# Kernel optimization log

Measured on AMD Instinct MI355X. Metric: run time of the kernel, lower is better.

Reference implementation:

```python
import jax, jax.numpy as jnp
import numpy as np
from jax import lax

RATIOS = (0.5, 1.0, 2.0)
SCALES = (8, 16, 32)
STRIDE = 16
N_ANCHOR = 9
N_PRE = 6000      # eval-mode n_pre_nms
N_POST = 300      # eval-mode n_post_nms
NMS_THRESH = 0.7
MIN_SIZE = 16.0


def _anchor_base():
    rows = []
    for r in RATIOS:
        for s in SCALES:
            h = STRIDE * s * np.sqrt(r)
            w = STRIDE * s * np.sqrt(1.0 / r)
            c = STRIDE / 2.0
            rows.append([c - h / 2.0, c - w / 2.0, c + h / 2.0, c + w / 2.0])
    return jnp.asarray(np.array(rows, np.float32))  # [9,4]


def _all_anchors(hh, ww):
    ab = _anchor_base()
    sy, sx = jnp.meshgrid(jnp.arange(hh) * STRIDE, jnp.arange(ww) * STRIDE, indexing='ij')
    shift = jnp.stack([sy.ravel(), sx.ravel(), sy.ravel(), sx.ravel()], axis=1).astype(jnp.float32)
    return (shift[:, None, :] + ab[None, :, :]).reshape(-1, 4)  # [hh*ww*9, 4]


def _conv(x, w, b, pad):
    y = lax.conv_general_dilated(x, w, (1, 1), ((pad, pad), (pad, pad)),
                                 dimension_numbers=('NCHW', 'OIHW', 'NCHW'))
    return y + b[None, :, None, None]


def _loc2bbox(anchor, loc):
    ah = anchor[:, 2] - anchor[:, 0]
    aw = anchor[:, 3] - anchor[:, 1]
    acy = anchor[:, 0] + 0.5 * ah
    acx = anchor[:, 1] + 0.5 * aw
    dy, dx, dh, dw = loc[:, 0], loc[:, 1], loc[:, 2], loc[:, 3]
    cy = dy * ah + acy
    cx = dx * aw + acx
    h = jnp.exp(dh) * ah
    w = jnp.exp(dw) * aw
    return jnp.stack([cy - 0.5 * h, cx - 0.5 * w, cy + 0.5 * h, cx + 0.5 * w], axis=1)


def _iou_matrix(boxes):
    tl = jnp.maximum(boxes[:, None, :2], boxes[None, :, :2])
    br = jnp.minimum(boxes[:, None, 2:], boxes[None, :, 2:])
    wh = jnp.clip(br - tl, 0.0)
    inter = wh[..., 0] * wh[..., 1]
    area = (boxes[:, 2] - boxes[:, 0]) * (boxes[:, 3] - boxes[:, 1])
    return inter / (area[:, None] + area[None, :] - inter + 1e-9)


def _nms_keep(boxes, valid):
    # boxes sorted by descending score; sequential greedy NMS via fori_loop.
    iou = _iou_matrix(boxes)
    idx = jnp.arange(boxes.shape[0])

    def body(i, keep):
        sup = keep[i] & (iou[i] > NMS_THRESH) & (idx > i)
        return keep & ~sup

    return lax.fori_loop(0, boxes.shape[0], body, valid)


def _proposals(loc, fg_score, anchors, img_h, img_w):
    boxes = _loc2bbox(anchors, loc)
    boxes = jnp.clip(boxes, 0.0, jnp.array([img_h, img_w, img_h, img_w], jnp.float32))
    hs = boxes[:, 2] - boxes[:, 0]
    ws = boxes[:, 3] - boxes[:, 1]
    valid = (hs >= MIN_SIZE) & (ws >= MIN_SIZE)
    score = jnp.where(valid, fg_score, -jnp.inf)
    topv, topi = lax.top_k(score, N_PRE)          # pre-NMS selection by score
    boxes = boxes[topi]
    keep = _nms_keep(boxes, topv > -jnp.inf)
    # compact first N_POST kept boxes (score order), zero-padded if fewer.
    rank = jnp.cumsum(keep) - 1
    pos = jnp.where(keep & (rank < N_POST), rank, N_POST)
    return jnp.zeros((N_POST + 1, 4), boxes.dtype).at[pos].set(boxes)[:N_POST]


def setup_inputs():
    key = jax.random.key(0)
    ks = jax.random.split(key, 4)
    C = 512
    return {
        'feature_map': jax.random.normal(ks[0], (2, C, 64, 64), jnp.float32),
        'conv1_w': jax.random.normal(ks[1], (C, C, 3, 3), jnp.float32) * 0.01,
        'conv1_b': jnp.zeros((C,), jnp.float32),
        'score_w': jax.random.normal(ks[2], (N_ANCHOR * 2, C, 1, 1), jnp.float32) * 0.01,
        'score_b': jnp.zeros((N_ANCHOR * 2,), jnp.float32),
        'loc_w': jax.random.normal(ks[3], (N_ANCHOR * 4, C, 1, 1), jnp.float32) * 0.01,
        'loc_b': jnp.zeros((N_ANCHOR * 4,), jnp.float32),
        'img_h': 1024,
        'img_w': 1024,
    }


def reference(feature_map, conv1_w, conv1_b, score_w, score_b, loc_w, loc_b, img_h, img_w):
    n, _, hh, ww = feature_map.shape
    h = jax.nn.relu(_conv(feature_map, conv1_w, conv1_b, 1))
    rpn_locs = _conv(h, loc_w, loc_b, 0).transpose(0, 2, 3, 1).reshape(n, -1, 4)
    scores_raw = _conv(h, score_w, score_b, 0).transpose(0, 2, 3, 1)  # [n,hh,ww,18]
    sm = jax.nn.softmax(scores_raw.reshape(n, hh, ww, N_ANCHOR, 2), axis=4)
    rpn_fg_scores = sm[..., 1].reshape(n, -1)
    rpn_scores = scores_raw.reshape(n, -1, 2)
    anchors = _all_anchors(hh, ww)
    rois = jax.vmap(lambda l, s: _proposals(l, s, anchors, img_h, img_w))(rpn_locs, rpn_fg_scores)
    roi_indices = jnp.repeat(jnp.arange(n, dtype=jnp.int32), N_POST)
    return rpn_locs, rpn_scores, rois.reshape(-1, 4), roi_indices, anchors
```

## Files before the change

### kernel.cpp

```cpp
#include <hip/hip_runtime.h>
#include <cmath>

#define NANCH 36864
#define NPRE 6000
#define NPOST 300

#define LOCS_OFF   0
#define SCORES_OFF 294912
#define ROIS_OFF   442368
#define RIDX_OFF   444768
#define ANCH_OFF   445368

#define WT_OFF      0ull
#define WTH_OFF     0ull
#define WTL_OFF     4718592ull
#define PREFIX_OFF  2097152ull
#define PREFIXM_OFF 2621440ull
#define SORTED_OFF  3145728ull
#define MASK_OFF    0ull
#define H_OFF       9437184ull
#define BOXES_OFF   26214400ull
#define W54_OFF     26214400ull
#define KEYS_OFF    27394048ull
#define HIST_OFF    27983872ull
#define SKEYS_OFF   28631168ull
#define SBOXES_OFF  28727168ull
#define VMASK_OFF   29033856ull
#define XTH_OFF     29360128ull
#define XTL_OFF     37748736ull
#define WS_NEED_MFMA 46137344ull

typedef _Float16 half8 __attribute__((ext_vector_type(8)));
typedef float floatx4 __attribute__((ext_vector_type(4)));

__device__ __forceinline__ void load_lds16(const float* g, float* l) {
#if __has_builtin(__builtin_amdgcn_global_load_lds)
  __builtin_amdgcn_global_load_lds(
      (const __attribute__((address_space(1))) void*)g,
      (__attribute__((address_space(3))) void*)l, 16, 0, 0);
#else
  int lane = threadIdx.x & 63;
  float4 v = *(const float4*)g;
  *(float4*)((char*)l + lane * 16) = v;
#endif
}

__device__ __forceinline__ void load_lds16g(const void* g, void* l) {
#if __has_builtin(__builtin_amdgcn_global_load_lds)
  __builtin_amdgcn_global_load_lds(
      (const __attribute__((address_space(1))) void*)g,
      (__attribute__((address_space(3))) void*)l, 16, 0, 0);
#else
  int lane = threadIdx.x & 63;
  float4 v = *(const float4*)g;
  *(float4*)((char*)l + lane * 16) = v;
#endif
}

__global__ __launch_bounds__(1024) void prep_kernel(
    const float* __restrict__ w, float* __restrict__ wt,
    const float* __restrict__ lw, const float* __restrict__ sw,
    float* __restrict__ w54p) {
  __shared__ float lds[9][32][33];
  if (blockIdx.x < 256) {
    int tx = threadIdx.x & 31;
    int ty = threadIdx.x >> 5;
    int ci0 = (blockIdx.x & 15) * 32;
    int co0 = (blockIdx.x >> 4) * 32;
    const float* src = w + ((size_t)(co0 + ty) * 512 + (ci0 + tx)) * 9;
#pragma unroll
    for (int k = 0; k < 9; k++) lds[k][tx][ty] = src[k];
    __syncthreads();
#pragma unroll
    for (int k = 0; k < 9; k++) {
      wt[((size_t)k * 512 + (ci0 + ty)) * 512 + co0 + tx] = lds[k][ty][tx];
    }
  } else {
    int t = (blockIdx.x - 256) * 1024 + threadIdx.x;
    int k = t >> 6, co = t & 63;
    float v = 0.f;
    if (co < 36) v = lw[(size_t)co * 512 + k];
    else if (co < 54) v = sw[(size_t)(co - 36) * 512 + k];
    w54p[t] = v;
  }
}

__global__ __launch_bounds__(1024) void prep16_kernel(
    const float* __restrict__ w, _Float16* __restrict__ wth,
    _Float16* __restrict__ wtl, const float* __restrict__ lw,
    const float* __restrict__ sw, float* __restrict__ w54p) {
  if (blockIdx.x < 256) {
    int tx = threadIdx.x & 31;
    int ty = threadIdx.x >> 5;
    int ci0 = (blockIdx.x & 15) * 32;
    int co0 = (blockIdx.x >> 4) * 32;
    const float* src = w + ((size_t)(co0 + ty) * 512 + (ci0 + tx)) * 9;
    size_t o = (size_t)(co0 + ty) * 512 + (ci0 + tx);
#pragma unroll
    for (int k = 0; k < 9; k++) {
      float v = src[k];
      _Float16 h = (_Float16)v;
      _Float16 l = (_Float16)((v - (float)h) * 1024.f);
      wth[(size_t)k * 262144 + o] = h;
      wtl[(size_t)k * 262144 + o] = l;
    }
  } else {
    int t = (blockIdx.x - 256) * 1024 + threadIdx.x;
    int k = t >> 6, co = t & 63;
    float v = 0.f;
    if (co < 36) v = lw[(size_t)co * 512 + k];
    else if (co < 54) v = sw[(size_t)(co - 36) * 512 + k];
    w54p[t] = v;
  }
}

__global__ __launch_bounds__(256) void prepx_kernel(
    const float* __restrict__ x, _Float16* __restrict__ xth,
    _Float16* __restrict__ xtl) {
  __shared__ float xs[32][65];
  int b = blockIdx.x;
  int cs = b & 15, ny = b >> 4;
  int n = ny >> 6, y = ny & 63;
  int tid = threadIdx.x;
  const float* xb = x + ((size_t)n << 21) + (y << 6);
#pragma unroll
  for (int p = 0; p < 8; p++) {
    int c = p * 4 + (tid >> 6);
    xs[c][tid & 63] = xb[((size_t)(cs * 32 + c) << 12) + (tid & 63)];
  }
  __syncthreads();
  int px = tid >> 2, cq = (tid & 3) * 8;
  unsigned int hw[4], lw2[4];
#pragma unroll
  for (int j = 0; j < 4; j++) {
    float v0 = xs[cq + 2 * j][px], v1 = xs[cq + 2 * j + 1][px];
    _Float16 h0 = (_Float16)v0, h1 = (_Float16)v1;
    _Float16 l0 = (_Float16)((v0 - (float)h0) * 1024.f);
    _Float16 l1 = (_Float16)((v1 - (float)h1) * 1024.f);
    hw[j] = (unsigned int)__builtin_bit_cast(unsigned short, h0) |
            ((unsigned int)__builtin_bit_cast(unsigned short, h1) << 16);
    lw2[j] = (unsigned int)__builtin_bit_cast(unsigned short, l0) |
             ((unsigned int)__builtin_bit_cast(unsigned short, l1) << 16);
  }
  size_t o = (size_t)b * 2048 + (size_t)px * 32 + cq;
  uint4 hv; hv.x = hw[0]; hv.y = hw[1]; hv.z = hw[2]; hv.w = hw[3];
  uint4 lv; lv.x = lw2[0]; lv.y = lw2[1]; lv.z = lw2[2]; lv.w = lw2[3];
  *(uint4*)(xth + o) = hv;
  *(uint4*)(xtl + o) = lv;
}

__global__ __launch_bounds__(256, 3) void conv1_mfma_kernel(
    const _Float16* __restrict__ xth, const _Float16* __restrict__ xtl,
    const _Float16* __restrict__ wth, const _Float16* __restrict__ wtl,
    const float* __restrict__ bias, float* __restrict__ hout) {
  __shared__ __align__(16) _Float16 sXh[6336];
  __shared__ __align__(16) _Float16 sXl[6336];
  __shared__ __align__(16) _Float16 sWh[4096];
  __shared__ __align__(16) _Float16 sWl[4096];
  int mb = blockIdx.x;
  int n = mb >> 6, y = mb & 63;
  int co0 = blockIdx.y << 7;
  int tid = threadIdx.x;
  int wv = tid >> 6, lane = tid & 63;
  int m15 = lane & 15, g = lane >> 4;

  floatx4 accm[2][4], accl[2][4];
#pragma unroll
  for (int ct = 0; ct < 2; ct++)
#pragma unroll
    for (int pt = 0; pt < 4; pt++) {
      accm[ct][pt] = (floatx4){0.f, 0.f, 0.f, 0.f};
      accl[ct][pt] = (floatx4){0.f, 0.f, 0.f, 0.f};
    }

  for (int t2 = tid; t2 < 3168; t2 += 256) {
    ((unsigned int*)sXh)[t2] = 0u;
    ((unsigned int*)sXl)[t2] = 0u;
  }
  __syncthreads();

  bool yv0 = (y > 0), yv2 = (y < 63);

  for (int cs = 0; cs < 16; cs++) {
    {
      int base = wv * 6;
#pragma unroll
      for (int i = 0; i < 6; i++) {
        int idx = base + i;
        int yr = idx >> 3, rem = idx & 7;
        int part = rem >> 2, d = rem & 3;
        int ys = y + yr - 1;
        if (ys >= 0 && ys < 64) {
          const _Float16* s =
              (part ? xtl : xth) +
              ((((size_t)(n * 64 + ys)) * 16 + cs) << 11) + (d << 9) +
              ((lane >> 2) << 5) + ((lane & 3) << 3);
          _Float16* dst = (part ? sXl : sXh) + yr * 2112 + 32 + (d << 9);
          load_lds16g(s, dst);
        }
      }
    }
    int ci0 = cs << 5;
    int p = wv >> 1, hf = wv & 1;
    const _Float16* wbase =
        (p ? wtl : wth) + (size_t)co0 * 512 + ci0 +
        ((size_t)(hf * 64 + (lane >> 2))) * 512 + ((lane & 3) << 3);
    _Float16* wdst0 = (p ? sWl : sWh) + (hf << 11);
#pragma unroll
    for (int tap = 0; tap < 9; tap++) {
      int ky = tap / 3;
      int kx = tap - ky * 3;
      if (ky == 0 && !yv0) continue;
      if (ky == 2 && !yv2) continue;
      const _Float16* ws = wbase + (size_t)tap * 262144;
#pragma unroll
      for (int d = 0; d < 4; d++)
        load_lds16g(ws + (size_t)d * 8192, wdst0 + (d << 9));
      __syncthreads();
      half8 Ah[2], Al[2], Bh[4], Bl[4];
#pragma unroll
      for (int ct = 0; ct < 2; ct++) {
        int ao = ((wv << 5) + (ct << 4) + m15) * 32 + (g << 3);
        Ah[ct] = *(const half8*)(sWh + ao);
        Al[ct] = *(const half8*)(sWl + ao);
      }
#pragma unroll
      for (int pt = 0; pt < 4; pt++) {
        int bo = ky * 2112 + ((pt << 4) + m15 + kx) * 32 + (g << 3);
        Bh[pt] = *(const half8*)(sXh + bo);
        Bl[pt] = *(const half8*)(sXl + bo);
      }
#pragma unroll
      for (int ct = 0; ct < 2; ct++)
#pragma unroll
        for (int pt = 0; pt < 4; pt++) {
          accm[ct][pt] = __builtin_amdgcn_mfma_f32_16x16x32_f16(
              Ah[ct], Bh[pt], accm[ct][pt], 0, 0, 0);
          accl[ct][pt] = __builtin_amdgcn_mfma_f32_16x16x32_f16(
              Ah[ct], Bl[pt], accl[ct][pt], 0, 0, 0);
          accl[ct][pt] = __builtin_amdgcn_mfma_f32_16x16x32_f16(
              Al[ct], Bh[pt], accl[ct][pt], 0, 0, 0);
        }
      __syncthreads();
    }
  }

#pragma unroll
  for (int ct = 0; ct < 2; ct++)
#pragma unroll
    for (int pt = 0; pt < 4; pt++) {
#pragma unroll
      for (int r = 0; r < 4; r++) {
        int co = co0 + (wv << 5) + (ct << 4) + (g << 2) + r;
        float v = accm[ct][pt][r] + accl[ct][pt][r] * 0.0009765625f +
                  bias[co];
        hout[((size_t)(n * 512 + co) << 12) + (y << 6) + (pt << 4) + m15] =
            fmaxf(v, 0.f);
      }
    }
}

__global__ __launch_bounds__(256) void conv1_kernel(
    const float* __restrict__ x, const float* __restrict__ wt,
    const float* __restrict__ bias, float* __restrict__ hout) {
  __shared__ __align__(16) float smem[10752];
  int mb = blockIdx.x;
  int n = mb >> 6, y = mb & 63;
  int co0 = blockIdx.y << 7;
  int tid = threadIdx.x;
  int team = tid >> 7;
  int tl = tid & 127;
  int cibase = team << 8;
  float* Asb = smem + team * 768;
  float* Bsb = smem + 1536 + team * 4608;
  int tx = tl & 7, ty = tl >> 3;
  int x0 = tx << 3;

  float acc[8][8];
#pragma unroll
  for (int j = 0; j < 8; j++)
#pragma unroll
    for (int i = 0; i < 8; i++) acc[j][i] = 0.f;

  const float* xb = x + ((size_t)n << 21);

  if (y == 0) {
    for (int t2 = tl; t2 < 256; t2 += 128) Asb[t2] = 0.f;
  }
  if (y == 63) {
    for (int t2 = tl; t2 < 256; t2 += 128) Asb[512 + t2] = 0.f;
  }

  int wv = tl >> 6;
  int lane = tl & 63;
  int lrow = lane >> 5;
  int lcol = (lane & 31) << 2;
  int aci = lane >> 4;
  int aoff = (lane & 15) << 2;

  for (int cc = 0; cc < 256; cc += 4) {
    int ci0 = cibase + cc;
    for (int yr = wv; yr < 3; yr += 2) {
      int ys = y + yr - 1;
      if (ys >= 0 && ys < 64) {
        const float* g =
            xb + (((size_t)(ci0 + aci)) << 12) + (ys << 6) + aoff;
        load_lds16(g, &Asb[yr << 8]);
      }
    }
    for (int i = 0; i < 9; i++) {
      int r0 = i * 4 + wv * 2;
      int row = r0 + lrow;
      int kk = row >> 2, ci = row & 3;
      const float* g = wt + (((size_t)(kk << 9)) + ci0 + ci) * 512 + co0 + lcol;
      load_lds16(g, &Bsb[r0 << 7]);
    }
    __syncthreads();
    for (int k = 0; k < 4; k++) {
#pragma unroll
      for (int ky = 0; ky < 3; ky++) {
        const float* arr = &Asb[((ky << 2) + k) << 6];
        float w10[10];
        w10[0] = (tx == 0) ? 0.f : arr[x0 - 1];
        float4 a0 = *(const float4*)&arr[x0];
        float4 a1 = *(const float4*)&arr[x0 + 4];
        w10[1] = a0.x; w10[2] = a0.y; w10[3] = a0.z; w10[4] = a0.w;
        w10[5] = a1.x; w10[6] = a1.y; w10[7] = a1.z; w10[8] = a1.w;
        w10[9] = (tx == 7) ? 0.f : arr[x0 + 8];
#pragma unroll
        for (int kx = 0; kx < 3; kx++) {
          int kk = ky * 3 + kx;
          const float* br = &Bsb[(((kk << 2) + k) << 7) + (ty << 3)];
          float4 b0 = *(const float4*)br;
          float4 b1 = *(const float4*)(br + 4);
          float bb[8] = {b0.x, b0.y, b0.z, b0.w, b1.x, b1.y, b1.z, b1.w};
#pragma unroll
          for (int j = 0; j < 8; j++)
#pragma unroll
            for (int dx = 0; dx < 8; dx++)
              acc[j][dx] = fmaf(w10[kx + dx], bb[j], acc[j][dx]);
        }
      }
    }
    __syncthreads();
  }

  if (team == 1) {
#pragma unroll
    for (int j = 0; j < 8; j++) {
      *(float4*)&smem[tl * 68 + (j << 3)] = *(float4*)&acc[j][0];
      *(float4*)&smem[tl * 68 + (j << 3) + 4] = *(float4*)&acc[j][4];
    }
  }
  __syncthreads();
  if (team == 0) {
#pragma unroll
    for (int j = 0; j < 8; j++) {
      int co = co0 + (ty << 3) + j;
      float bv = bias[co];
      float4 p0 = *(float4*)&smem[tl * 68 + (j << 3)];
      float4 p1 = *(float4*)&smem[tl * 68 + (j << 3) + 4];
      float4 v0, v1;
      v0.x = fmaxf((acc[j][0] + p0.x) + bv, 0.f);
      v0.y = fmaxf((acc[j][1] + p0.y) + bv, 0.f);
      v0.z = fmaxf((acc[j][2] + p0.z) + bv, 0.f);
      v0.w = fmaxf((acc[j][3] + p0.w) + bv, 0.f);
      v1.x = fmaxf((acc[j][4] + p1.x) + bv, 0.f);
      v1.y = fmaxf((acc[j][5] + p1.y) + bv, 0.f);
      v1.z = fmaxf((acc[j][6] + p1.z) + bv, 0.f);
      v1.w = fmaxf((acc[j][7] + p1.w) + bv, 0.f);
      float* o = &hout[(((size_t)(n * 512 + co)) << 12) + (y << 6) + x0];
      *(float4*)o = v0;
      *(float4*)(o + 4) = v1;
    }
  }
}

__global__ __launch_bounds__(256) void heads_kernel(
    const float* __restrict__ h, const float* __restrict__ w54p,
    const float* __restrict__ loc_b, const float* __restrict__ score_b,
    float* __restrict__ out) {
  __shared__ __align__(16) float hs[32 * 64];
  __shared__ __align__(16) float wsd[32 * 64];
  __shared__ float sacc[64 * 65];
  int n = blockIdx.x >> 6;
  int p0 = (blockIdx.x & 63) << 6;
  int tid = threadIdx.x;
  int txp = tid & 63;
  int tw = tid >> 6;
  float acc[16];
#pragma unroll
  for (int j = 0; j < 16; j++) acc[j] = 0.f;
  const float* hb = h + ((size_t)n * 512) * 4096 + p0;
  for (int k0 = 0; k0 < 512; k0 += 32) {
    for (int t = tid; t < 512; t += 256) {
      int r = t >> 4, l = (t & 15) << 2;
      *(float4*)&hs[(r << 6) + l] =
          *(const float4*)&hb[(((size_t)(k0 + r)) << 12) + l];
      *(float4*)&wsd[(r << 6) + l] =
          *(const float4*)&w54p[((k0 + r) << 6) + l];
    }
    __syncthreads();
    for (int k = 0; k < 32; k++) {
      float hv = hs[(k << 6) + txp];
      const float* wr = &wsd[(k << 6) + (tw << 4)];
#pragma unroll
      for (int u = 0; u < 4; u++) {
        float4 wv = *(const float4*)(wr + (u << 2));
        acc[u * 4 + 0] = fmaf(hv, wv.x, acc[u * 4 + 0]);
        acc[u * 4 + 1] = fmaf(hv, wv.y, acc[u * 4 + 1]);
        acc[u * 4 + 2] = fmaf(hv, wv.z, acc[u * 4 + 2]);
        acc[u * 4 + 3] = fmaf(hv, wv.w, acc[u * 4 + 3]);
      }
    }
    __syncthreads();
  }
#pragma unroll
  for (int j = 0; j < 16; j++) sacc[(tw * 16 + j) * 65 + txp] = acc[j];
  __syncthreads();
  for (int t = tid; t < 64 * 54; t += 256) {
    int p = t / 54, c = t - p * 54;
    float v = sacc[c * 65 + p];
    int gp = (n << 12) + p0 + p;
    if (c < 36) out[LOCS_OFF + (size_t)gp * 36 + c] = v + loc_b[c];
    else out[SCORES_OFF + (size_t)gp * 18 + (c - 36)] = v + score_b[c - 36];
  }
}

__global__ void decode_kernel(const float* __restrict__ out_ro,
                              const int* __restrict__ pimh,
                              const int* __restrict__ pimw,
                              float* __restrict__ boxes,
                              unsigned long long* __restrict__ keys,
                              unsigned int* __restrict__ hist,
                              float* __restrict__ out) {
  int t = blockIdx.x * 256 + threadIdx.x;
  int n = t / NANCH, k = t - n * NANCH;
  float imh = (float)pimh[0], imw = (float)pimw[0];

  int a = k % 9, pos = k / 9;
  int jj = pos & 63, ii = pos >> 6;
  int ridx = a / 3, sidx = a % 3;
  double r = (ridx == 0) ? 0.5 : ((ridx == 1) ? 1.0 : 2.0);
  double s = (sidx == 0) ? 8.0 : ((sidx == 1) ? 16.0 : 32.0);
  double ahh = 16.0 * s * sqrt(r);
  double aww = 16.0 * s * sqrt(1.0 / r);
  float b0 = (float)(8.0 - ahh / 2.0), b1 = (float)(8.0 - aww / 2.0);
  float b2 = (float)(8.0 + ahh / 2.0), b3 = (float)(8.0 + aww / 2.0);
  float sy = (float)(ii * 16), sx = (float)(jj * 16);
  float a0 = sy + b0, a1 = sx + b1, a2 = sy + b2, a3 = sx + b3;
  if (n == 0) {
    float* o = out + ANCH_OFF + (size_t)k * 4;
    o[0] = a0; o[1] = a1; o[2] = a2; o[3] = a3;
  }

  const float* loc = out_ro + LOCS_OFF + (size_t)t * 4;
  const float* sc = out_ro + SCORES_OFF + (size_t)t * 2;
  float ah = __fsub_rn(a2, a0), aw = __fsub_rn(a3, a1);
  float acy = __fadd_rn(a0, 0.5f * ah), acx = __fadd_rn(a1, 0.5f * aw);
  float dy = loc[0], dx = loc[1], dh = loc[2], dw = loc[3];
  float cy = __fadd_rn(__fmul_rn(dy, ah), acy);
  float cx = __fadd_rn(__fmul_rn(dx, aw), acx);
  float hh = __fmul_rn(expf(dh), ah);
  float ww = __fmul_rn(expf(dw), aw);
  float y1 = __fsub_rn(cy, 0.5f * hh), x1 = __fsub_rn(cx, 0.5f * ww);
  float y2 = __fadd_rn(cy, 0.5f * hh), x2 = __fadd_rn(cx, 0.5f * ww);
  y1 = fminf(fmaxf(y1, 0.f), imh); x1 = fminf(fmaxf(x1, 0.f), imw);
  y2 = fminf(fmaxf(y2, 0.f), imh); x2 = fminf(fmaxf(x2, 0.f), imw);
  bool valid = (__fsub_rn(y2, y1) >= 16.f) && (__fsub_rn(x2, x1) >= 16.f);
  float s0 = sc[0], s1 = sc[1];
  float m = fmaxf(s0, s1);
  float e0 = expf(__fsub_rn(s0, m)), e1 = expf(__fsub_rn(s1, m));
  float fg = __fdiv_rn(e1, __fadd_rn(e0, e1));
  float score = valid ? fg : -INFINITY;
  unsigned int u = __float_as_uint(score);
  unsigned int ord = (u & 0x80000000u) ? ~u : (u | 0x80000000u);
  unsigned long long key =
      ((unsigned long long)(~ord) << 16) | (unsigned long long)(k & 0xFFFF);
  float4 b4; b4.x = y1; b4.y = x1; b4.z = y2; b4.w = x2;
  *(float4*)(boxes + (size_t)t * 4) = b4;
  keys[t] = key;
  if (valid)
    atomicAdd(&hist[((size_t)n << 16) + (unsigned int)(key >> 32)], 1u);
}

__global__ __launch_bounds__(1024) void scanfull_kernel(
    const unsigned int* __restrict__ hist, unsigned int* __restrict__ prefix,
    unsigned int* __restrict__ prefix_mut) {
  int n = blockIdx.x;
  const uint4* h4 = (const uint4*)(hist + ((size_t)n << 16));
  uint4* pf4 = (uint4*)(prefix + ((size_t)n << 16));
  uint4* pm4 = (uint4*)(prefix_mut + ((size_t)n << 16));
  __shared__ unsigned int ps[1024];
  int tid = threadIdx.x;
  int base4 = tid << 4;
  uint4 vals[16];
  unsigned int s = 0;
#pragma unroll
  for (int i = 0; i < 16; i++) {
    vals[i] = h4[base4 + i];
    s += vals[i].x + vals[i].y + vals[i].z + vals[i].w;
  }
  ps[tid] = s;
  __syncthreads();
  for (int off = 1; off < 1024; off <<= 1) {
    unsigned int v = ps[tid];
    unsigned int add = (tid >= off) ? ps[tid - off] : 0u;
    __syncthreads();
    ps[tid] = v + add;
    __syncthreads();
  }
  unsigned int run = ps[tid] - s;
#pragma unroll
  for (int i = 0; i < 16; i++) {
    uint4 hv = vals[i];
    uint4 pv;
    pv.x = run; run += hv.x;
    pv.y = run; run += hv.y;
    pv.z = run; run += hv.z;
    pv.w = run; run += hv.w;
    pf4[base4 + i] = pv;
    pm4[base4 + i] = pv;
  }
}

__global__ void scatter_kernel(const unsigned long long* __restrict__ keys,
                               unsigned int* __restrict__ prefix_mut,
                               unsigned long long* __restrict__ sorted) {
  int t = blockIdx.x * 256 + threadIdx.x;
  int n = t / NANCH;
  unsigned long long key = keys[t];
  unsigned int b = (unsigned int)(key >> 32);
  if (b >= 0xFF80u) return;
  unsigned int pos = atomicAdd(&prefix_mut[((size_t)n << 16) + b], 1u);
  if (pos < 8192) sorted[((size_t)n << 13) + pos] = key;
}

__global__ void fixup_kernel(const unsigned long long* __restrict__ sorted,
                             const unsigned int* __restrict__ prefix,
                             const unsigned int* __restrict__ hist,
                             const float* __restrict__ boxes,
                             unsigned long long* __restrict__ skeys,
                             float* __restrict__ sboxes) {
  int t = blockIdx.x * 256 + threadIdx.x;
  int n = t / 7168;
  int s = t - n * 7168;
  const unsigned long long* srt = sorted + ((size_t)n << 13);
  unsigned long long key = srt[s];
  unsigned int hi = (unsigned int)(key >> 16);
  if (hi >= 0xFF800000u) {
    if (s < NPRE) skeys[(size_t)n * NPRE + s] = key;
    return;
  }
  unsigned int b = (unsigned int)(key >> 32);
  unsigned int st = prefix[((size_t)n << 16) + b];
  if (st >= (unsigned)NPRE) return;
  unsigned int cnt = hist[((size_t)n << 16) + b];
  unsigned int r = 0;
  if (cnt > 1) {
    for (unsigned int j = 0; j < cnt; j++) r += (srt[st + j] < key) ? 1u : 0u;
  }
  unsigned int pos = st + r;
  if (pos < (unsigned)NPRE) {
    skeys[(size_t)n * NPRE + pos] = key;
    int k = (int)(key & 0xFFFFull);
    float4 bx = *(const float4*)(boxes + (((size_t)n * NANCH) + k) * 4);
    *(float4*)(sboxes + ((size_t)n * NPRE + pos) * 4) = bx;
  }
}

__global__ __launch_bounds__(64) void nms_mask_kernel(
    const float* __restrict__ sboxes,
    const unsigned long long* __restrict__ skeys,
    unsigned long long* __restrict__ vmask,
    unsigned long long* __restrict__ mask) {
  int n = blockIdx.z;
  int ib = blockIdx.x, jb = blockIdx.y;
  if (jb < ib) return;
  int lane = threadIdx.x;
  __shared__ __align__(16) float jbox[64][4];
  int j = jb * 64 + lane;
  float4 bj4 = (j < NPRE)
                   ? *(const float4*)(sboxes + ((size_t)n * NPRE + j) * 4)
                   : float4{0.f, 0.f, 0.f, 0.f};
  *(float4*)jbox[lane] = bj4;
  __syncthreads();
  if (jb == ib) {
    int idx = ib * 64 + lane;
    bool ok = false;
    if (idx < NPRE) {
      unsigned int khi = (unsigned int)(skeys[(size_t)n * NPRE + idx] >> 16);
      ok = khi < 0xFF800000u;
    }
    unsigned long long m = __ballot(ok);
    if (lane == 0) vmask[(size_t)n * 94 + ib] = m;
  }
  int i = ib * 64 + lane;
  if (i >= NPRE) return;
  float4 bi = *(const float4*)(sboxes + ((size_t)n * NPRE + i) * 4);
  float ay1 = bi.x, ax1 = bi.y, ay2 = bi.z, ax2 = bi.w;
  float areaA = __fmul_rn(__fsub_rn(ay2, ay1), __fsub_rn(ax2, ax1));
  unsigned long long bits = 0ull;
#pragma unroll 8
  for (int l = 0; l < 64; l++) {
    float4 bj = *(const float4*)jbox[l];
    float ty1 = fmaxf(ay1, bj.x), tx1 = fmaxf(ax1, bj.y);
    float ty2 = fminf(ay2, bj.z), tx2 = fminf(ax2, bj.w);
    float wh0 = fmaxf(__fsub_rn(ty2, ty1), 0.f);
    float wh1 = fmaxf(__fsub_rn(tx2, tx1), 0.f);
    float inter = __fmul_rn(wh0, wh1);
    float areaB = __fmul_rn(__fsub_rn(bj.z, bj.x), __fsub_rn(bj.w, bj.y));
    float den = __fadd_rn(__fsub_rn(__fadd_rn(areaA, areaB), inter), 1e-9f);
    float iou = __fdiv_rn(inter, den);
    if (iou > 0.7f) bits |= (1ull << l);
  }
  mask[((size_t)n * NPRE + i) * 94 + jb] = bits;
}

__global__ __launch_bounds__(64) void nms_reduce_kernel(
    const unsigned long long* __restrict__ mask,
    const unsigned long long* __restrict__ vmask,
    const float* __restrict__ sboxes, float* __restrict__ out) {
  int n = blockIdx.x;
  int lane = threadIdx.x;
  __shared__ int kept[NPOST];
  __shared__ int s_count;

  unsigned long long rlo = ~vmask[(size_t)n * 94 + lane];
  unsigned long long rhi = (64 + lane < 94) ? ~vmask[(size_t)n * 94 + 64 + lane]
                                            : ~0ull;
  int count = 0;
  for (int c = 0; c < 94 && count < NPOST; c++) {
    unsigned long long curw =
        (c < 64) ? __shfl(rlo, c) : __shfl(rhi, c - 64);
    unsigned long long cand = ~curw;
    while (cand != 0ull && count < NPOST) {
      int b = __builtin_ctzll(cand);
      int i = c * 64 + b;
      if (lane == 0) kept[count] = i;
      count++;
      const unsigned long long* row = mask + ((size_t)n * NPRE + i) * 94;
      unsigned long long r0 = row[lane];
      unsigned long long r1 = (64 + lane < 94) ? row[64 + lane] : 0ull;
      rlo |= r0; rhi |= r1;
      curw = (c < 64) ? __shfl(rlo, c) : __shfl(rhi, c - 64);
      cand = ~curw;
      cand &= (b == 63) ? 0ull : (~0ull << (b + 1));
    }
  }
  if (lane == 0) s_count = count;
  __syncthreads();
  count = s_count;

  float* rois = out + ROIS_OFF + (size_t)n * NPOST * 4;
  float* ridx = out + RIDX_OFF + (size_t)n * NPOST;
  for (int s = lane; s < NPOST; s += 64) {
    float4 v = {0.f, 0.f, 0.f, 0.f};
    if (s < count) {
      int i = kept[s];
      v = *(const float4*)(sboxes + ((size_t)n * NPRE + i) * 4);
    }
    *(float4*)(rois + (size_t)s * 4) = v;
    ridx[s] = (float)n;
  }
}

extern "C" void kernel_launch(void* const* d_in, const int* in_sizes, int n_in,
                              void* d_out, int out_size, void* d_ws,
                              size_t ws_size, hipStream_t stream) {
  const float* feat = (const float*)d_in[0];
  const float* w1 = (const float*)d_in[1];
  const float* b1 = (const float*)d_in[2];
  const float* sw = (const float*)d_in[3];
  const float* sb = (const float*)d_in[4];
  const float* lw = (const float*)d_in[5];
  const float* lb = (const float*)d_in[6];
  const int* pimh = (const int*)d_in[7];
  const int* pimw = (const int*)d_in[8];
  float* out = (float*)d_out;
  char* ws = (char*)d_ws;

  float* wt = (float*)(ws + WT_OFF);
  _Float16* wth = (_Float16*)(ws + WTH_OFF);
  _Float16* wtl = (_Float16*)(ws + WTL_OFF);
  _Float16* xth = (_Float16*)(ws + XTH_OFF);
  _Float16* xtl = (_Float16*)(ws + XTL_OFF);
  float* w54p = (float*)(ws + W54_OFF);
  float* hbuf = (float*)(ws + H_OFF);
  float* boxes = (float*)(ws + BOXES_OFF);
  unsigned long long* keys = (unsigned long long*)(ws + KEYS_OFF);
  unsigned int* hist = (unsigned int*)(ws + HIST_OFF);
  unsigned int* prefix = (unsigned int*)(ws + PREFIX_OFF);
  unsigned int* prefix_mut = (unsigned int*)(ws + PREFIXM_OFF);
  unsigned long long* sorted = (unsigned long long*)(ws + SORTED_OFF);
  unsigned long long* skeys = (unsigned long long*)(ws + SKEYS_OFF);
  float* sboxes = (float*)(ws + SBOXES_OFF);
  unsigned long long* vmask = (unsigned long long*)(ws + VMASK_OFF);
  unsigned long long* nmask = (unsigned long long*)(ws + MASK_OFF);

  hipMemsetAsync(ws + HIST_OFF, 0, 524288, stream);
  hipMemsetAsync(ws + SORTED_OFF, 0xFF, 131072, stream);

  bool big = (ws_size >= WS_NEED_MFMA);
  if (big) {
    prep16_kernel<<<288, 1024, 0, stream>>>(w1, wth, wtl, lw, sw, w54p);
    prepx_kernel<<<2048, 256, 0, stream>>>(feat, xth, xtl);
    conv1_mfma_kernel<<<dim3(128, 4), 256, 0, stream>>>(xth, xtl, wth, wtl,
                                                        b1, hbuf);
  } else {
    prep_kernel<<<288, 1024, 0, stream>>>(w1, wt, lw, sw, w54p);
    conv1_kernel<<<dim3(128, 4), 256, 0, stream>>>(feat, wt, b1, hbuf);
  }
  heads_kernel<<<128, 256, 0, stream>>>(hbuf, w54p, lb, sb, out);
  decode_kernel<<<288, 256, 0, stream>>>(out, pimh, pimw, boxes, keys, hist,
                                         out);
  scanfull_kernel<<<2, 1024, 0, stream>>>(hist, prefix, prefix_mut);
  scatter_kernel<<<288, 256, 0, stream>>>(keys, prefix_mut, sorted);
  fixup_kernel<<<56, 256, 0, stream>>>(sorted, prefix, hist, boxes, skeys,
                                       sboxes);
  nms_mask_kernel<<<dim3(94, 94, 2), 64, 0, stream>>>(sboxes, skeys, vmask,
                                                      nmask);
  nms_reduce_kernel<<<2, 64, 0, stream>>>(nmask, vmask, sboxes, out);
}
```

Baseline: 631.8 us.

## Prefetch upcoming NMS mask rows speculatively in the sequential reduce loop

Rewrites the greedy NMS reduce loop so it keeps up to four candidate surviving boxes ahead and issues their suppression-row loads early. Candidates are found with wave ballots over the removed bitmask. Any speculative candidate that a newly kept box kills is recomputed and reloaded. The goal is to hide global-memory latency on the serial dependency chain of row loads, at the cost of extra ballot and shuffle work per step and occasional wasted loads.

New measurement: 769.9 us. 1.22x slower.

```diff
diff --git a/kernel.cpp b/kernel.cpp
--- a/kernel.cpp
+++ b/kernel.cpp
@@ -617,6 +617,61 @@
   mask[((size_t)n * NPRE + i) * 94 + jb] = bits;
 }
 
+#define QINV (1 << 30)
+
+__device__ __forceinline__ unsigned long long nms_word_at(
+    unsigned long long rlo, unsigned long long rhi, int w) {
+  unsigned long long lo = __shfl(rlo, w & 63);
+  unsigned long long hi = __shfl(rhi, (w - 64) & 63);
+  return (w < 64) ? lo : hi;
+}
+
+__device__ __forceinline__ int nms_next_alive(unsigned long long rlo,
+                                              unsigned long long rhi,
+                                              int lane, int pfrom) {
+  int w0 = pfrom >> 6, b0 = pfrom & 63;
+  unsigned long long mylo = ~rlo;
+  if (lane < w0) mylo = 0ull;
+  else if (lane == w0) mylo &= (~0ull << b0);
+  int l2 = lane + 64;
+  unsigned long long myhi = (l2 < 94) ? ~rhi : 0ull;
+  if (l2 < w0) myhi = 0ull;
+  else if (l2 == w0) myhi &= (~0ull << b0);
+  unsigned long long blo = __ballot(mylo != 0ull);
+  unsigned long long bhi = __ballot(myhi != 0ull);
+  int w;
+  unsigned long long wv;
+  if (blo) {
+    w = (int)__builtin_ctzll(blo);
+    wv = __shfl(mylo, w);
+  } else if (bhi) {
+    int wl = (int)__builtin_ctzll(bhi);
+    w = 64 + wl;
+    wv = __shfl(myhi, wl);
+  } else {
+    return QINV;
+  }
+  return (w << 6) + (int)__builtin_ctzll(wv);
+}
+
+__device__ __forceinline__ void nms_load_row(
+    const unsigned long long* __restrict__ mask, size_t nbase, int q,
+    int lane, unsigned long long& r0, unsigned long long& r1) {
+  if (q < QINV) {
+    const unsigned long long* row = mask + (nbase + (size_t)q) * 94;
+    r0 = row[lane];
+    r1 = (64 + lane < 94) ? row[64 + lane] : 0ull;
+  } else {
+    r0 = 0ull;
+    r1 = 0ull;
+  }
+}
+
+__device__ __forceinline__ bool nms_dead(unsigned long long rlo,
+                                         unsigned long long rhi, int q) {
+  return ((nms_word_at(rlo, rhi, q >> 6) >> (q & 63)) & 1ull) != 0ull;
+}
+
 __global__ __launch_bounds__(64) void nms_reduce_kernel(
     const unsigned long long* __restrict__ mask,
     const unsigned long long* __restrict__ vmask,
@@ -625,28 +680,49 @@
   int lane = threadIdx.x;
   __shared__ int kept[NPOST];
   __shared__ int s_count;
+  size_t nbase = (size_t)n * NPRE;
 
   unsigned long long rlo = ~vmask[(size_t)n * 94 + lane];
   unsigned long long rhi = (64 + lane < 94) ? ~vmask[(size_t)n * 94 + 64 + lane]
                                             : ~0ull;
+
+  int q0 = nms_next_alive(rlo, rhi, lane, 0);
+  int q1 = (q0 == QINV) ? QINV : nms_next_alive(rlo, rhi, lane, q0 + 1);
+  int q2 = (q1 == QINV) ? QINV : nms_next_alive(rlo, rhi, lane, q1 + 1);
+  int q3 = (q2 == QINV) ? QINV : nms_next_alive(rlo, rhi, lane, q2 + 1);
+  unsigned long long a0, c0, a1, c1, a2, c2, a3, c3;
+  nms_load_row(mask, nbase, q0, lane, a0, c0);
+  nms_load_row(mask, nbase, q1, lane, a1, c1);
+  nms_load_row(mask, nbase, q2, lane, a2, c2);
+  nms_load_row(mask, nbase, q3, lane, a3, c3);
+
   int count = 0;
-  for (int c = 0; c < 94 && count < NPOST; c++) {
-    unsigned long long curw =
-        (c < 64) ? __shfl(rlo, c) : __shfl(rhi, c - 64);
-    unsigned long long cand = ~curw;
-    while (cand != 0ull && count < NPOST) {
-      int b = __builtin_ctzll(cand);
-      int i = c * 64 + b;
-      if (lane == 0) kept[count] = i;
-      count++;
-      const unsigned long long* row = mask + ((size_t)n * NPRE + i) * 94;
-      unsigned long long r0 = row[lane];
-      unsigned long long r1 = (64 + lane < 94) ? row[64 + lane] : 0ull;
-      rlo |= r0; rhi |= r1;
-      curw = (c < 64) ? __shfl(rlo, c) : __shfl(rhi, c - 64);
-      cand = ~curw;
-      cand &= (b == 63) ? 0ull : (~0ull << (b + 1));
-    }
+  while (q0 != QINV && count < NPOST) {
+    if (lane == 0) kept[count] = q0;
+    count++;
+    rlo |= a0;
+    rhi |= c0;
+    if (q1 != QINV && nms_dead(rlo, rhi, q1)) {
+      q1 = nms_next_alive(rlo, rhi, lane, q0 + 1);
+      q2 = (q1 == QINV) ? QINV : nms_next_alive(rlo, rhi, lane, q1 + 1);
+      q3 = (q2 == QINV) ? QINV : nms_next_alive(rlo, rhi, lane, q2 + 1);
+      nms_load_row(mask, nbase, q1, lane, a1, c1);
+      nms_load_row(mask, nbase, q2, lane, a2, c2);
+      nms_load_row(mask, nbase, q3, lane, a3, c3);
+    } else if (q2 != QINV && nms_dead(rlo, rhi, q2)) {
+      q2 = nms_next_alive(rlo, rhi, lane, q1 + 1);
+      q3 = (q2 == QINV) ? QINV : nms_next_alive(rlo, rhi, lane, q2 + 1);
+      nms_load_row(mask, nbase, q2, lane, a2, c2);
+      nms_load_row(mask, nbase, q3, lane, a3, c3);
+    } else if (q3 != QINV && nms_dead(rlo, rhi, q3)) {
+      q3 = nms_next_alive(rlo, rhi, lane, q2 + 1);
+      nms_load_row(mask, nbase, q3, lane, a3, c3);
+    }
+    q0 = q1; a0 = a1; c0 = c1;
+    q1 = q2; a1 = a2; c1 = c2;
+    q2 = q3; a2 = a3; c2 = c3;
+    q3 = (q2 == QINV) ? QINV : nms_next_alive(rlo, rhi, lane, q2 + 1);
+    nms_load_row(mask, nbase, q3, lane, a3, c3);
   }
   if (lane == 0) s_count = count;
   __syncthreads();
```
